# Performance work log

Measured on AMD Instinct MI355X. Metric: run time of the kernel, lower is better.

## Reference

```python
import jax, jax.numpy as jnp
import numpy as np

BATCH = 4
N_MELS, T_LEN, PATCH = 128, 512, 16
D_MODEL, D_INNER, D_STATE, DT_RANK, D_CONV = 512, 1024, 16, 32, 4
DEPTH, N_CLASSES = 4, 10


def _silu(x):
    return x * jax.nn.sigmoid(x)


def _ln(x, w, b):
    m = x.mean(-1, keepdims=True)
    v = ((x - m) ** 2).mean(-1, keepdims=True)
    return (x - m) * jax.lax.rsqrt(v + 1e-5) * w + b


def _causal_conv(x, w, b):
    # x: (B, L, D); w: (D, K) depthwise causal conv (mamba conv1d)
    K, L = w.shape[-1], x.shape[1]
    xp = jnp.pad(x, ((0, 0), (K - 1, 0), (0, 0)))
    y = sum(xp[:, k:k + L, :] * w[:, k] for k in range(K))
    return y + b


def _ssm(xc, conv_w, conv_b, xproj_w, dtproj_w, dtproj_b, A_log, Dp):
    # One directional selective scan (mamba S6).
    u = _silu(_causal_conv(xc, conv_w, conv_b))              # (B,L,Di)
    xdbl = jnp.einsum('bld,ed->ble', u, xproj_w)             # (B,L,dt_rank+2S)
    dtr, Bm, Cm = jnp.split(xdbl, [DT_RANK, DT_RANK + D_STATE], axis=-1)
    dt = jax.nn.softplus(jnp.einsum('blr,dr->bld', dtr, dtproj_w) + dtproj_b)
    A = -jnp.exp(A_log)                                      # (Di,S)
    dA = jnp.exp(dt[..., None] * A)                          # (B,L,Di,S)
    dBu = (dt * u)[..., None] * Bm[:, :, None, :]            # (B,L,Di,S)

    def comb(e1, e2):
        a1, b1 = e1
        a2, b2 = e2
        return a1 * a2, a2 * b1 + b2

    _, h = jax.lax.associative_scan(comb, (dA, dBu), axis=1)  # parallel linear recurrence
    return jnp.einsum('blds,bls->bld', h, Cm) + u * Dp


def _forward(x, patch_w, patch_b, in_proj_w, conv_w_f, conv_b_f, conv_w_b, conv_b_b,
             xproj_w_f, xproj_w_b, dtproj_w_f, dtproj_b_f, dtproj_w_b, dtproj_b_b,
             A_log_f, A_log_b, D_f, D_b, out_proj_w, norm_w, norm_b,
             normf_w, normf_b, ln_w, ln_b, fc1_w, fc1_b, fc2_w, fc2_b):
    B = x.shape[0]
    # Patch embed: conv with kernel == stride -> reshape + einsum
    xp = x.reshape(B, 1, N_MELS // PATCH, PATCH, T_LEN // PATCH, PATCH)
    tok = jnp.einsum('bchpwq,dcpq->bhwd', xp, patch_w) + patch_b
    h = tok.reshape(B, -1, D_MODEL)                           # (B, 256, D)
    for i in range(DEPTH):
        xn = _ln(h, norm_w[i], norm_b[i])
        xz = jnp.einsum('bld,ed->ble', xn, in_proj_w[i])
        xc, z = jnp.split(xz, 2, axis=-1)
        y_f = _ssm(xc, conv_w_f[i], conv_b_f[i], xproj_w_f[i],
                   dtproj_w_f[i], dtproj_b_f[i], A_log_f[i], D_f[i])
        y_b = jnp.flip(_ssm(jnp.flip(xc, 1), conv_w_b[i], conv_b_b[i], xproj_w_b[i],
                            dtproj_w_b[i], dtproj_b_b[i], A_log_b[i], D_b[i]), 1)
        y = (y_f + y_b) * _silu(z)                            # bimamba v2: fwd + flipped bwd, gated
        h = h + jnp.einsum('bld,ed->ble', y, out_proj_w[i])
    h = _ln(h, normf_w, normf_b)
    feat = h.mean(axis=1)                                     # pooled features (B, D)
    c = _ln(feat, ln_w, ln_b)
    c = jnp.maximum(c @ fc1_w.T + fc1_b, 0.0)
    return c @ fc2_w.T + fc2_b


def setup_inputs() -> dict:
    ks = iter(jax.random.split(jax.random.key(0), 64))

    def rn(shape, s=0.02):
        return jax.random.normal(next(ks), shape, jnp.float32) * s

    inp = {}
    inp['x'] = jax.random.normal(next(ks), (BATCH, 1, N_MELS, T_LEN), jnp.float32)
    inp['patch_w'] = rn((D_MODEL, 1, PATCH, PATCH))
    inp['patch_b'] = jnp.zeros((D_MODEL,), jnp.float32)
    inp['in_proj_w'] = rn((DEPTH, 2 * D_INNER, D_MODEL))
    A_init = jnp.log(jnp.tile(jnp.arange(1, D_STATE + 1, dtype=jnp.float32), (DEPTH, D_INNER, 1)))
    for sfx in ('f', 'b'):
        inp[f'conv_w_{sfx}'] = rn((DEPTH, D_INNER, D_CONV), 0.2)
        inp[f'conv_b_{sfx}'] = jnp.zeros((DEPTH, D_INNER), jnp.float32)
        inp[f'xproj_w_{sfx}'] = rn((DEPTH, DT_RANK + 2 * D_STATE, D_INNER))
        inp[f'dtproj_w_{sfx}'] = rn((DEPTH, D_INNER, DT_RANK), 0.1)
        inp[f'dtproj_b_{sfx}'] = jnp.full((DEPTH, D_INNER), -4.6, jnp.float32)  # softplus -> dt ~ 0.01
        inp[f'A_log_{sfx}'] = A_init
        inp[f'D_{sfx}'] = jnp.ones((DEPTH, D_INNER), jnp.float32)
    inp['out_proj_w'] = rn((DEPTH, D_MODEL, D_INNER))
    inp['norm_w'] = jnp.ones((DEPTH, D_MODEL), jnp.float32)
    inp['norm_b'] = jnp.zeros((DEPTH, D_MODEL), jnp.float32)
    inp['normf_w'] = jnp.ones((D_MODEL,), jnp.float32)
    inp['normf_b'] = jnp.zeros((D_MODEL,), jnp.float32)
    inp['ln_w'] = jnp.ones((D_MODEL,), jnp.float32)
    inp['ln_b'] = jnp.zeros((D_MODEL,), jnp.float32)
    inp['fc1_w'] = rn((512, D_MODEL))
    inp['fc1_b'] = jnp.zeros((512,), jnp.float32)
    inp['fc2_w'] = rn((N_CLASSES, 512))
    inp['fc2_b'] = jnp.zeros((N_CLASSES,), jnp.float32)
    return inp


def reference(x, patch_w, patch_b, in_proj_w, conv_w_f, conv_b_f, conv_w_b, conv_b_b,
              xproj_w_f, xproj_w_b, dtproj_w_f, dtproj_b_f, dtproj_w_b, dtproj_b_b,
              A_log_f, A_log_b, D_f, D_b, out_proj_w, norm_w, norm_b,
              normf_w, normf_b, ln_w, ln_b, fc1_w, fc1_b, fc2_w, fc2_b):
    return _forward(x, patch_w, patch_b, in_proj_w, conv_w_f, conv_b_f, conv_w_b, conv_b_b,
                    xproj_w_f, xproj_w_b, dtproj_w_f, dtproj_b_f, dtproj_w_b, dtproj_b_b,
                    A_log_f, A_log_b, D_f, D_b, out_proj_w, norm_w, norm_b,
                    normf_w, normf_b, ln_w, ln_b, fc1_w, fc1_b, fc2_w, fc2_b)
```

## Files before the change

### kernel.cpp

```cpp
#include <hip/hip_runtime.h>


#define BB 4
#define LL 256
#define DM 512
#define DI 1024

typedef unsigned short u16;
typedef unsigned int u32;
typedef __attribute__((ext_vector_type(8))) short s8v;
typedef __attribute__((ext_vector_type(4))) float f4v;

__device__ __forceinline__ float silu_f(float x){ return x/(1.f+__expf(-x)); }
__device__ __forceinline__ float b2f(u16 u){
  union { u32 i; float f; } v; v.i = ((u32)u) << 16; return v.f;
}
__device__ __forceinline__ u16 f2bf(float f){
  union { float f; u32 u; } v; v.f = f;
  u32 r = (v.u + 0x7fffu + ((v.u >> 16) & 1u)) >> 16;
  return (u16)r;
}
__device__ __forceinline__ void split8(const float* f, s8v& hi, s8v& lo){
#pragma unroll
  for (int j = 0; j < 8; ++j){
    u16 h = f2bf(f[j]);
    float hf = b2f(h);
    hi[j] = (short)h;
    lo[j] = (short)f2bf(f[j] - hf);
  }
}

__device__ __forceinline__ float row_sum16(float p){
  union { float f; int i; } v, r;
  v.f = p;
  r.i = __builtin_amdgcn_update_dpp(0, v.i, 0x111, 0xF, 0xF, true); v.f += r.f;
  r.i = __builtin_amdgcn_update_dpp(0, v.i, 0x112, 0xF, 0xF, true); v.f += r.f;
  r.i = __builtin_amdgcn_update_dpp(0, v.i, 0x114, 0xF, 0xF, true); v.f += r.f;
  r.i = __builtin_amdgcn_update_dpp(0, v.i, 0x118, 0xF, 0xF, true); v.f += r.f;
  return v.f;
}

__device__ __forceinline__ void block_reduce2(float& a, float& b, float* sc, int nw){
  int lane = threadIdx.x & 63, wid = threadIdx.x >> 6;
#pragma unroll
  for (int o = 32; o > 0; o >>= 1){
    a += __shfl_down(a, o, 64);
    b += __shfl_down(b, o, 64);
  }
  if (lane == 0){ sc[wid*2] = a; sc[wid*2+1] = b; }
  __syncthreads();
  float ta = 0.f, tb = 0.f;
  for (int i = 0; i < nw; ++i){ ta += sc[i*2]; tb += sc[i*2+1]; }
  a = ta; b = tb;
}

__global__ __launch_bounds__(256) void convert_w(const float* __restrict__ inW,
    const float* __restrict__ outW, u16* __restrict__ inHi, u16* __restrict__ inLo,
    u16* __restrict__ outHi, u16* __restrict__ outLo){
  int idx = blockIdx.x*256 + threadIdx.x;
  const float4* src; ushort4* dh; ushort4* dl;
  if (idx < 262144){
    src = (const float4*)inW + idx;
    dh = (ushort4*)inHi + idx; dl = (ushort4*)inLo + idx;
  } else {
    int j = idx - 262144;
    src = (const float4*)outW + j;
    dh = (ushort4*)outHi + j; dl = (ushort4*)outLo + j;
  }
  float4 v = *src;
  ushort4 h, l;
  h.x = f2bf(v.x); l.x = f2bf(v.x - b2f(h.x));
  h.y = f2bf(v.y); l.y = f2bf(v.y - b2f(h.y));
  h.z = f2bf(v.z); l.z = f2bf(v.z - b2f(h.z));
  h.w = f2bf(v.w); l.w = f2bf(v.w - b2f(h.w));
  *dh = h; *dl = l;
}

__global__ __launch_bounds__(256) void patch_embed(const float* __restrict__ x,
    const float* __restrict__ pw, const float* __restrict__ pb, float* __restrict__ h){
  __shared__ float xs[8*256];
  int blk = blockIdx.x;
  int b = blk >> 6, ph = (blk >> 3) & 7, pg = (blk >> 1) & 3, dh = blk & 1;
  int t = threadIdx.x;
  for (int idx = t; idx < 2048; idx += 256){
    int j = idx >> 8, pix = idx & 255, p = pix >> 4, q = pix & 15;
    xs[idx] = x[(size_t)(b*128 + ph*16 + p)*512 + pg*128 + j*16 + q];
  }
  __syncthreads();
  int d = dh*256 + t;
  float acc[8] = {};
  const float* wr = pw + (size_t)d*256;
  for (int i = 0; i < 256; i += 8){
    float4 w0 = *(const float4*)(wr + i);
    float4 w1 = *(const float4*)(wr + i + 4);
    float wf[8] = {w0.x,w0.y,w0.z,w0.w,w1.x,w1.y,w1.z,w1.w};
#pragma unroll
    for (int j = 0; j < 8; ++j){
#pragma unroll
      for (int jj = 0; jj < 8; ++jj)
        acc[j] = fmaf(xs[j*256 + i + jj], wf[jj], acc[j]);
    }
  }
  float bias = pb[d];
#pragma unroll
  for (int j = 0; j < 8; ++j)
    h[(size_t)(b*256 + ph*32 + pg*8 + j)*512 + d] = acc[j] + bias;
}

__global__ __launch_bounds__(256) void gemm1_ln_mfma(const float* __restrict__ X,
    const float* __restrict__ lnw, const float* __restrict__ lnb, int lnOff,
    const u16* __restrict__ Whi, const u16* __restrict__ Wlo, float* __restrict__ C){
  __shared__ __align__(16) u16 Ah[2048], Al[2048], Bh[2048], Bl[2048];
  __shared__ float rmean[64], rrstd[64];
  int bm = blockIdx.y*64, bn = blockIdx.x*64;
  int t = threadIdx.x;
  int sr = t >> 2, sc = (t & 3)*8;
  {
    const float* xr = X + (size_t)(bm + sr)*512 + (t & 3)*128;
    float s = 0.f, ss = 0.f;
    for (int i = 0; i < 128; i += 4){
      float4 v = *(const float4*)(xr + i);
      s  += v.x + v.y + v.z + v.w;
      ss += v.x*v.x + v.y*v.y + v.z*v.z + v.w*v.w;
    }
    s += __shfl_xor(s, 1, 64); ss += __shfl_xor(ss, 1, 64);
    s += __shfl_xor(s, 2, 64); ss += __shfl_xor(ss, 2, 64);
    if ((t & 3) == 0){
      float m = s * (1.f/512.f);
      float var = ss * (1.f/512.f) - m*m;
      rmean[sr] = m; rrstd[sr] = rsqrtf(var + 1e-5f);
    }
  }
  __syncthreads();
  float mm = rmean[sr], rr = rrstd[sr];
  int lane = t & 63, wv = t >> 6, ml = lane & 15, quad = lane >> 4;
  int mq = wv >> 1, nq = wv & 1;
  f4v acc[2][2] = {};
  for (int k0 = 0; k0 < 512; k0 += 32){
    const float* xr = X + (size_t)(bm + sr)*512 + k0 + sc;
    float4 a0 = *(const float4*)xr;
    float4 a1 = *(const float4*)(xr + 4);
    float4 g0 = *(const float4*)(lnw + lnOff + k0 + sc);
    float4 g1 = *(const float4*)(lnw + lnOff + k0 + sc + 4);
    float4 c0 = *(const float4*)(lnb + lnOff + k0 + sc);
    float4 c1 = *(const float4*)(lnb + lnOff + k0 + sc + 4);
    float af[8] = {
      (a0.x-mm)*rr*g0.x + c0.x, (a0.y-mm)*rr*g0.y + c0.y,
      (a0.z-mm)*rr*g0.z + c0.z, (a0.w-mm)*rr*g0.w + c0.w,
      (a1.x-mm)*rr*g1.x + c1.x, (a1.y-mm)*rr*g1.y + c1.y,
      (a1.z-mm)*rr*g1.z + c1.z, (a1.w-mm)*rr*g1.w + c1.w };
    s8v ahv, alv; split8(af, ahv, alv);
    *(s8v*)&Ah[sr*32 + sc] = ahv;
    *(s8v*)&Al[sr*32 + sc] = alv;
    uint4 bhv = *(const uint4*)(Whi + (size_t)(bn + sr)*512 + k0 + sc);
    uint4 blv = *(const uint4*)(Wlo + (size_t)(bn + sr)*512 + k0 + sc);
    *(uint4*)&Bh[sr*32 + sc] = bhv;
    *(uint4*)&Bl[sr*32 + sc] = blv;
    __syncthreads();
    s8v ah[2], al2[2], bh2[2], bl2[2];
#pragma unroll
    for (int mt = 0; mt < 2; ++mt){
      int row = mq*32 + mt*16 + ml;
      ah[mt]  = *(s8v*)&Ah[row*32 + quad*8];
      al2[mt] = *(s8v*)&Al[row*32 + quad*8];
    }
#pragma unroll
    for (int nt = 0; nt < 2; ++nt){
      int col = nq*32 + nt*16 + ml;
      bh2[nt] = *(s8v*)&Bh[col*32 + quad*8];
      bl2[nt] = *(s8v*)&Bl[col*32 + quad*8];
    }
#pragma unroll
    for (int mt = 0; mt < 2; ++mt)
#pragma unroll
      for (int nt = 0; nt < 2; ++nt){
        acc[mt][nt] = __builtin_amdgcn_mfma_f32_16x16x32_bf16(ah[mt],  bh2[nt], acc[mt][nt], 0, 0, 0);
        acc[mt][nt] = __builtin_amdgcn_mfma_f32_16x16x32_bf16(al2[mt], bh2[nt], acc[mt][nt], 0, 0, 0);
        acc[mt][nt] = __builtin_amdgcn_mfma_f32_16x16x32_bf16(ah[mt],  bl2[nt], acc[mt][nt], 0, 0, 0);
      }
    __syncthreads();
  }
#pragma unroll
  for (int mt = 0; mt < 2; ++mt)
#pragma unroll
    for (int nt = 0; nt < 2; ++nt)
#pragma unroll
      for (int r = 0; r < 4; ++r)
        C[(size_t)(bm + mq*32 + mt*16 + quad*4 + r)*2048 + bn + nq*32 + nt*16 + ml] =
            acc[mt][nt][r];
}

__global__ __launch_bounds__(256) void gemm2_gate_mfma(const float* __restrict__ yb2,
    const float* __restrict__ xz, const u16* __restrict__ Whi,
    const u16* __restrict__ Wlo, float* __restrict__ C){
  __shared__ __align__(16) u16 Ah[2048], Al[2048], Bh[2048], Bl[2048];
  int bm = blockIdx.y*64, bn = blockIdx.x*64;
  int t = threadIdx.x;
  int sr = t >> 2, sc = (t & 3)*8;
  int lane = t & 63, wv = t >> 6, ml = lane & 15, quad = lane >> 4;
  int mq = wv >> 1, nq = wv & 1;
  f4v acc[2][2] = {};
  for (int k0 = 0; k0 < 1024; k0 += 32){
    int m = bm + sr;
    const float* fp = yb2 + (size_t)m*DI + k0 + sc;
    const float* rp = yb2 + (size_t)(1024 + m)*DI + k0 + sc;
    const float* zp = xz + (size_t)m*2048 + 1024 + k0 + sc;
    float4 f0 = *(const float4*)fp,       f1 = *(const float4*)(fp + 4);
    float4 r0 = *(const float4*)rp,       r1 = *(const float4*)(rp + 4);
    float4 z0 = *(const float4*)zp,       z1 = *(const float4*)(zp + 4);
    float af[8] = {
      (f0.x+r0.x)*silu_f(z0.x), (f0.y+r0.y)*silu_f(z0.y),
      (f0.z+r0.z)*silu_f(z0.z), (f0.w+r0.w)*silu_f(z0.w),
      (f1.x+r1.x)*silu_f(z1.x), (f1.y+r1.y)*silu_f(z1.y),
      (f1.z+r1.z)*silu_f(z1.z), (f1.w+r1.w)*silu_f(z1.w) };
    s8v ahv, alv; split8(af, ahv, alv);
    *(s8v*)&Ah[sr*32 + sc] = ahv;
    *(s8v*)&Al[sr*32 + sc] = alv;
    uint4 bhv = *(const uint4*)(Whi + (size_t)(bn + sr)*1024 + k0 + sc);
    uint4 blv = *(const uint4*)(Wlo + (size_t)(bn + sr)*1024 + k0 + sc);
    *(uint4*)&Bh[sr*32 + sc] = bhv;
    *(uint4*)&Bl[sr*32 + sc] = blv;
    __syncthreads();
    s8v ah[2], al2[2], bh2[2], bl2[2];
#pragma unroll
    for (int mt = 0; mt < 2; ++mt){
      int row = mq*32 + mt*16 + ml;
      ah[mt]  = *(s8v*)&Ah[row*32 + quad*8];
      al2[mt] = *(s8v*)&Al[row*32 + quad*8];
    }
#pragma unroll
    for (int nt = 0; nt < 2; ++nt){
      int col = nq*32 + nt*16 + ml;
      bh2[nt] = *(s8v*)&Bh[col*32 + quad*8];
      bl2[nt] = *(s8v*)&Bl[col*32 + quad*8];
    }
#pragma unroll
    for (int mt = 0; mt < 2; ++mt)
#pragma unroll
      for (int nt = 0; nt < 2; ++nt){
        acc[mt][nt] = __builtin_amdgcn_mfma_f32_16x16x32_bf16(ah[mt],  bh2[nt], acc[mt][nt], 0, 0, 0);
        acc[mt][nt] = __builtin_amdgcn_mfma_f32_16x16x32_bf16(al2[mt], bh2[nt], acc[mt][nt], 0, 0, 0);
        acc[mt][nt] = __builtin_amdgcn_mfma_f32_16x16x32_bf16(ah[mt],  bl2[nt], acc[mt][nt], 0, 0, 0);
      }
    __syncthreads();
  }
#pragma unroll
  for (int mt = 0; mt < 2; ++mt)
#pragma unroll
    for (int nt = 0; nt < 2; ++nt)
#pragma unroll
      for (int r = 0; r < 4; ++r){
        float* cp = C + (size_t)(bm + mq*32 + mt*16 + quad*4 + r)*512 +
                    bn + nq*32 + nt*16 + ml;
        *cp += acc[mt][nt][r];
      }
}

__global__ __launch_bounds__(256) void fused_cxd(const float* __restrict__ xz,
    const float* __restrict__ cwF, const float* __restrict__ cbF,
    const float* __restrict__ cwB, const float* __restrict__ cbB,
    const float* __restrict__ xwF, const float* __restrict__ xwB,
    const float* __restrict__ dtwF, const float* __restrict__ dtbF,
    const float* __restrict__ dtwB, const float* __restrict__ dtbB,
    int cwOff, int cbOff, int xwOff, int dtwOff, int dtbOff,
    float* __restrict__ u, float* __restrict__ xdbl, float* __restrict__ dtout){
  __shared__ float us[4*1024];
  __shared__ float part[16*64];
  __shared__ float dtr[4*32];
  int blk = blockIdx.x;
  int dir = blk >> 8, rem = blk & 255, b = rem >> 6, lg = rem & 63;
  int l0 = lg*4;
  const float* cw  = dir ? cwB  : cwF;
  const float* cb  = dir ? cbB  : cbF;
  const float* xw  = dir ? xwB  : xwF;
  const float* dtw = dir ? dtwB : dtwF;
  const float* dtb = dir ? dtbB : dtbF;
  int t = threadIdx.x;
  int rbase = (dir*BB + b)*LL;
  for (int dd = 0; dd < 4; ++dd){
    int d = t + dd*256;
    float4 w4 = *(const float4*)(cw + cwOff + d*4);
    float wf[4] = {w4.x, w4.y, w4.z, w4.w};
    float bias = cb[cbOff + d];
#pragma unroll
    for (int r = 0; r < 4; ++r){
      int l = l0 + r;
      float acc = bias;
#pragma unroll
      for (int k = 0; k < 4; ++k){
        int li = l + k - 3;
        if (li >= 0){
          int sl = dir ? (LL-1-li) : li;
          acc = fmaf(xz[(size_t)(b*LL + sl)*2048 + d], wf[k], acc);
        }
      }
      float uval = silu_f(acc);
      us[r*1024 + d] = uval;
      u[(size_t)(rbase + l)*DI + d] = uval;
    }
  }
  __syncthreads();
  {
    int e = t & 63, pr = t >> 6;
    float accs[4] = {};
    const float* wr = xw + xwOff + (size_t)e*1024 + pr*256;
    for (int i = 0; i < 256; i += 8){
      float4 w0 = *(const float4*)(wr + i);
      float4 w1 = *(const float4*)(wr + i + 4);
      float wf[8] = {w0.x,w0.y,w0.z,w0.w,w1.x,w1.y,w1.z,w1.w};
#pragma unroll
      for (int r = 0; r < 4; ++r){
        const float* ub = us + r*1024 + pr*256 + i;
#pragma unroll
        for (int j = 0; j < 8; ++j)
          accs[r] = fmaf(ub[j], wf[j], accs[r]);
      }
    }
#pragma unroll
    for (int r = 0; r < 4; ++r) part[(pr*4 + r)*64 + e] = accs[r];
  }
  __syncthreads();
  {
    int r = t >> 6, e = t & 63;
    float v = part[(0*4+r)*64+e] + part[(1*4+r)*64+e] +
              part[(2*4+r)*64+e] + part[(3*4+r)*64+e];
    xdbl[(size_t)(rbase + l0 + r)*64 + e] = v;
    if (e < 32) dtr[r*32 + e] = v;
  }
  __syncthreads();
  for (int dd = 0; dd < 4; ++dd){
    int d = t + dd*256;
    float bias = dtb[dtbOff + d];
    float accs[4] = {bias, bias, bias, bias};
    const float* wr = dtw + dtwOff + (size_t)d*32;
    for (int i = 0; i < 32; i += 8){
      float4 w0 = *(const float4*)(wr + i);
      float4 w1 = *(const float4*)(wr + i + 4);
      float wf[8] = {w0.x,w0.y,w0.z,w0.w,w1.x,w1.y,w1.z,w1.w};
#pragma unroll
      for (int r = 0; r < 4; ++r)
#pragma unroll
        for (int j = 0; j < 8; ++j)
          accs[r] = fmaf(dtr[r*32 + i + j], wf[j], accs[r]);
    }
#pragma unroll
    for (int r = 0; r < 4; ++r){
      float sv = accs[r];
      dtout[(size_t)(rbase + l0 + r)*DI + d] = (sv > 15.f) ? sv : log1pf(__expf(sv));
    }
  }
}

__global__ __launch_bounds__(256) void scan_coal(const float* __restrict__ dt,
    const float* __restrict__ u, const float* __restrict__ xd,
    const float* __restrict__ AlogF, const float* __restrict__ AlogB,
    const float* __restrict__ DF, const float* __restrict__ DB,
    int aOff, int dOff, float* __restrict__ y){
  __shared__ __align__(16) float dtuT[16][516];
  __shared__ __align__(16) float BCT[16][516];
  __shared__ __align__(16) float ytile[128][16];
  int blk = blockIdx.x;
  int dir = blk >> 8, b = (blk >> 6) & 3, dg = blk & 63;
  int t = threadIdx.x;
  int rbase = (dir*BB + b)*LL;
  const float* Alog = dir ? AlogB : AlogF;
  const float* Dpt  = dir ? DB : DF;
  {
    int q = t & 3, lb = t >> 2;
    for (int pass = 0; pass < 4; ++pass){
      int l = pass*64 + lb;
      float4 dv = *(const float4*)(dt + (size_t)(rbase + l)*DI + dg*16 + q*4);
      float4 uv = *(const float4*)(u  + (size_t)(rbase + l)*DI + dg*16 + q*4);
      float2 p0 = {dv.x, uv.x}, p1 = {dv.y, uv.y}, p2 = {dv.z, uv.z}, p3 = {dv.w, uv.w};
      *(float2*)&dtuT[q*4+0][l*2] = p0;
      *(float2*)&dtuT[q*4+1][l*2] = p1;
      *(float2*)&dtuT[q*4+2][l*2] = p2;
      *(float2*)&dtuT[q*4+3][l*2] = p3;
    }
  }
  {
    int h8 = t & 7, lb = t >> 3;
    for (int pass = 0; pass < 8; ++pass){
      int l = pass*32 + lb;
      float4 v = *(const float4*)(xd + (size_t)(rbase + l)*64 + 32 + h8*4);
      if (h8 < 4){
        int s0 = h8*4;
        BCT[s0+0][l*2] = v.x; BCT[s0+1][l*2] = v.y;
        BCT[s0+2][l*2] = v.z; BCT[s0+3][l*2] = v.w;
      } else {
        int s0 = (h8-4)*4;
        BCT[s0+0][l*2+1] = v.x; BCT[s0+1][l*2+1] = v.y;
        BCT[s0+2][l*2+1] = v.z; BCT[s0+3][l*2+1] = v.w;
      }
    }
  }
  int s = t & 15, dl = t >> 4;
  float Av = -__expf(Alog[aOff + dg*256 + t]);
  float Dp = Dpt[dOff + dg*16 + dl];
  __syncthreads();
  float h = 0.f;
  for (int half = 0; half < 2; ++half){
    for (int l0 = half*128; l0 < half*128 + 128; l0 += 4){
      float4 du01 = *(const float4*)&dtuT[dl][l0*2];
      float4 du23 = *(const float4*)&dtuT[dl][l0*2 + 4];
      float4 bc01 = *(const float4*)&BCT[s][l0*2];
      float4 bc23 = *(const float4*)&BCT[s][l0*2 + 4];
      float dtv[4] = {du01.x, du01.z, du23.x, du23.z};
      float uv[4]  = {du01.y, du01.w, du23.y, du23.w};
      float Bv[4]  = {bc01.x, bc01.z, bc23.x, bc23.z};
      float Cv[4]  = {bc01.y, bc01.w, bc23.y, bc23.w};
#pragma unroll
      for (int i = 0; i < 4; ++i){
        float a = __expf(dtv[i] * Av);
        h = fmaf(a, h, dtv[i]*uv[i]*Bv[i]);
        float p = h * Cv[i];
        float sum = row_sum16(p);
        if (s == 15){
          int lr = (l0 + i) & 127;
          ytile[lr][dl] = fmaf(uv[i], Dp, sum);
        }
      }
    }
    __syncthreads();
    {
      int d4 = t & 3, lh = t >> 2;
      for (int pass = 0; pass < 2; ++pass){
        int lr = pass*64 + lh;
        int l = half*128 + lr;
        int lo = dir ? (255 - l) : l;
        float4 vv = *(const float4*)&ytile[lr][d4*4];
        *(float4*)(y + (size_t)(rbase + lo)*DI + dg*16 + d4*4) = vv;
      }
    }
    __syncthreads();
  }
}

__global__ __launch_bounds__(256) void ln_kernel(const float* __restrict__ x,
    const float* __restrict__ w, const float* __restrict__ bias,
    float* __restrict__ y){
  __shared__ float sc[8];
  int row = blockIdx.x, t = threadIdx.x;
  const float* xr = x + (size_t)row*DM;
  float v0 = xr[t], v1 = xr[t + 256];
  float s = v0 + v1, ss = v0*v0 + v1*v1;
  block_reduce2(s, ss, sc, 4);
  float mean = s * (1.f/512.f);
  float var = ss * (1.f/512.f) - mean*mean;
  float inv = rsqrtf(var + 1e-5f);
  float* yr = y + (size_t)row*DM;
  yr[t]       = (v0 - mean)*inv*w[t]       + bias[t];
  yr[t + 256] = (v1 - mean)*inv*w[t + 256] + bias[t + 256];
}

__global__ __launch_bounds__(256) void pool_kernel(const float* __restrict__ hn,
    float* __restrict__ feat){
  __shared__ float part[4][64];
  int b = blockIdx.x >> 3, dg = blockIdx.x & 7;
  int t = threadIdx.x, dl = t & 63, lq = t >> 6;
  const float* p = hn + (size_t)(b*256 + lq*64)*512 + dg*64 + dl;
  float s = 0.f;
#pragma unroll 4
  for (int i = 0; i < 64; ++i) s += p[(size_t)i*512];
  part[lq][dl] = s;
  __syncthreads();
  if (t < 64)
    feat[b*512 + dg*64 + t] =
        (part[0][t] + part[1][t] + part[2][t] + part[3][t]) * (1.f/256.f);
}

__global__ __launch_bounds__(512) void head_kernel(const float* __restrict__ feat,
    const float* __restrict__ lnw, const float* __restrict__ lnb,
    const float* __restrict__ fc1w, const float* __restrict__ fc1b,
    const float* __restrict__ fc2w, const float* __restrict__ fc2b,
    float* __restrict__ out){
  __shared__ float sc[16];
  __shared__ float cbuf[512];
  __shared__ float rbuf[512];
  int b = blockIdx.x, t = threadIdx.x;
  float v = feat[b*512 + t];
  float s = v, ss = v*v;
  block_reduce2(s, ss, sc, 8);
  float mean = s * (1.f/512.f);
  float var = ss * (1.f/512.f) - mean*mean;
  float inv = rsqrtf(var + 1e-5f);
  cbuf[t] = (v - mean)*inv*lnw[t] + lnb[t];
  __syncthreads();
  float a = fc1b[t];
  const float* w1 = fc1w + (size_t)t*512;
  for (int i = 0; i < 512; i += 8){
    float4 w0 = *(const float4*)(w1 + i);
    float4 w4 = *(const float4*)(w1 + i + 4);
    float wf[8] = {w0.x,w0.y,w0.z,w0.w,w4.x,w4.y,w4.z,w4.w};
#pragma unroll
    for (int j = 0; j < 8; ++j) a = fmaf(cbuf[i + j], wf[j], a);
  }
  rbuf[t] = fmaxf(a, 0.f);
  __syncthreads();
  if (t < 10){
    float a2 = fc2b[t];
    const float* w2 = fc2w + (size_t)t*512;
    for (int i = 0; i < 512; ++i) a2 = fmaf(rbuf[i], w2[i], a2);
    out[b*10 + t] = a2;
  }
}

extern "C" void kernel_launch(void* const* d_in, const int* in_sizes, int n_in,
                              void* d_out, int out_size, void* d_ws, size_t ws_size,
                              hipStream_t stream) {
  (void)in_sizes; (void)n_in; (void)out_size; (void)ws_size;
  const float* x          = (const float*)d_in[0];
  const float* patch_w    = (const float*)d_in[1];
  const float* patch_b    = (const float*)d_in[2];
  const float* in_proj_w  = (const float*)d_in[3];
  const float* conv_w_f   = (const float*)d_in[4];
  const float* conv_b_f   = (const float*)d_in[5];
  const float* xproj_w_f  = (const float*)d_in[6];
  const float* dtproj_w_f = (const float*)d_in[7];
  const float* dtproj_b_f = (const float*)d_in[8];
  const float* A_log_f    = (const float*)d_in[9];
  const float* D_f        = (const float*)d_in[10];
  const float* conv_w_b   = (const float*)d_in[11];
  const float* conv_b_b   = (const float*)d_in[12];
  const float* xproj_w_b  = (const float*)d_in[13];
  const float* dtproj_w_b = (const float*)d_in[14];
  const float* dtproj_b_b = (const float*)d_in[15];
  const float* A_log_b    = (const float*)d_in[16];
  const float* D_b        = (const float*)d_in[17];
  const float* out_proj_w = (const float*)d_in[18];
  const float* norm_w     = (const float*)d_in[19];
  const float* norm_b     = (const float*)d_in[20];
  const float* normf_w    = (const float*)d_in[21];
  const float* normf_b    = (const float*)d_in[22];
  const float* ln_w       = (const float*)d_in[23];
  const float* ln_b       = (const float*)d_in[24];
  const float* fc1_w      = (const float*)d_in[25];
  const float* fc1_b      = (const float*)d_in[26];
  const float* fc2_w      = (const float*)d_in[27];
  const float* fc2_b      = (const float*)d_in[28];

  float* ws   = (float*)d_ws;
  float* hbuf = ws;
  float* xz   = ws + 524288;
  float* ubuf = ws + 2621440;
  float* xdbl = ws + 4718592;
  float* dtb  = ws + 4849664;
  float* ybuf = ws + 6946816;
  float* hn   = ws + 9043968;
  u16*   inHi = (u16*)(ws + 9568256);
  u16*   inLo = (u16*)(ws + 10092544);
  u16*   outHi= (u16*)(ws + 10616832);
  u16*   outLo= (u16*)(ws + 10878976);
  float* feat = ws + 11141120;

  patch_embed<<<256, 256, 0, stream>>>(x, patch_w, patch_b, hbuf);
  for (int i = 0; i < 4; ++i){
    convert_w<<<1536, 256, 0, stream>>>(in_proj_w + (size_t)i*1048576,
                                        out_proj_w + (size_t)i*524288,
                                        inHi, inLo, outHi, outLo);
    gemm1_ln_mfma<<<dim3(32, 16), 256, 0, stream>>>(
        hbuf, norm_w, norm_b, i*512, inHi, inLo, xz);
    fused_cxd<<<512, 256, 0, stream>>>(
        xz, conv_w_f, conv_b_f, conv_w_b, conv_b_b, xproj_w_f, xproj_w_b,
        dtproj_w_f, dtproj_b_f, dtproj_w_b, dtproj_b_b,
        i*4096, i*1024, i*65536, i*32768, i*1024, ubuf, xdbl, dtb);
    scan_coal<<<512, 256, 0, stream>>>(
        dtb, ubuf, xdbl, A_log_f, A_log_b, D_f, D_b, i*16384, i*1024, ybuf);
    gemm2_gate_mfma<<<dim3(8, 16), 256, 0, stream>>>(
        ybuf, xz, outHi, outLo, hbuf);
  }
  ln_kernel<<<1024, 256, 0, stream>>>(hbuf, normf_w, normf_b, hn);
  pool_kernel<<<32, 256, 0, stream>>>(hn, feat);
  head_kernel<<<4, 512, 0, stream>>>(feat, ln_w, ln_b, fc1_w, fc1_b, fc2_w, fc2_b,
                                     (float*)d_out);
}
```

Measured before the change: 756.4 us.

## Split LN and gate prologues into prep kernels, share padded-LDS bf16 GEMM

The LayerNorm and the SiLU gate, along with the hi/lo bf16 split, move out of the two MFMA GEMMs into separate row-wise prep kernels that write bf16 hi/lo activations to workspace. A single generic gemm_bf16 kernel then loads pre-split operands straight into LDS, whose row stride is padded to 40 elements to reduce bank conflicts. This removes the redundant per-tile LN and gate math and bf16 conversion that was repeated across every N-tile block. The cost is two extra launches per layer and an extra round trip of the activations through global memory.

```diff
diff --git a/kernel.cpp b/kernel.cpp
--- a/kernel.cpp
+++ b/kernel.cpp
@@ -5,6 +5,7 @@
 #define LL 256
 #define DM 512
 #define DI 1024
+#define LDST 40
 
 typedef unsigned short u16;
 typedef unsigned int u32;
@@ -19,15 +20,6 @@
   union { float f; u32 u; } v; v.f = f;
   u32 r = (v.u + 0x7fffu + ((v.u >> 16) & 1u)) >> 16;
   return (u16)r;
-}
-__device__ __forceinline__ void split8(const float* f, s8v& hi, s8v& lo){
-#pragma unroll
-  for (int j = 0; j < 8; ++j){
-    u16 h = f2bf(f[j]);
-    float hf = b2f(h);
-    hi[j] = (short)h;
-    lo[j] = (short)f2bf(f[j] - hf);
-  }
 }
 
 __device__ __forceinline__ float row_sum16(float p){
@@ -107,68 +99,76 @@
     h[(size_t)(b*256 + ph*32 + pg*8 + j)*512 + d] = acc[j] + bias;
 }
 
-__global__ __launch_bounds__(256) void gemm1_ln_mfma(const float* __restrict__ X,
-    const float* __restrict__ lnw, const float* __restrict__ lnb, int lnOff,
-    const u16* __restrict__ Whi, const u16* __restrict__ Wlo, float* __restrict__ C){
-  __shared__ __align__(16) u16 Ah[2048], Al[2048], Bh[2048], Bl[2048];
-  __shared__ float rmean[64], rrstd[64];
+__global__ __launch_bounds__(256) void prep_ln(const float* __restrict__ x,
+    const float* __restrict__ w, const float* __restrict__ bias, int wOff,
+    u16* __restrict__ hiO, u16* __restrict__ loO){
+  __shared__ float sc[8];
+  int row = blockIdx.x, t = threadIdx.x;
+  const float* xr = x + (size_t)row*DM;
+  float v0 = xr[t], v1 = xr[t + 256];
+  float s = v0 + v1, ss = v0*v0 + v1*v1;
+  block_reduce2(s, ss, sc, 4);
+  float mean = s * (1.f/512.f);
+  float var = ss * (1.f/512.f) - mean*mean;
+  float inv = rsqrtf(var + 1e-5f);
+  float o0 = (v0 - mean)*inv*w[wOff + t]       + bias[wOff + t];
+  float o1 = (v1 - mean)*inv*w[wOff + t + 256] + bias[wOff + t + 256];
+  u16 h0 = f2bf(o0), h1 = f2bf(o1);
+  hiO[(size_t)row*DM + t]       = h0;
+  hiO[(size_t)row*DM + t + 256] = h1;
+  loO[(size_t)row*DM + t]       = f2bf(o0 - b2f(h0));
+  loO[(size_t)row*DM + t + 256] = f2bf(o1 - b2f(h1));
+}
+
+__global__ __launch_bounds__(256) void prep_gate(const float* __restrict__ ybuf,
+    const float* __restrict__ xz, u16* __restrict__ gHi, u16* __restrict__ gLo){
+  int row = blockIdx.x, t = threadIdx.x;
+  int c = t*4;
+  float4 yf = *(const float4*)(ybuf + (size_t)row*DI + c);
+  float4 yb = *(const float4*)(ybuf + 1048576 + (size_t)row*DI + c);
+  float4 zv = *(const float4*)(xz + (size_t)row*2048 + 1024 + c);
+  float g0 = (yf.x + yb.x)*silu_f(zv.x);
+  float g1 = (yf.y + yb.y)*silu_f(zv.y);
+  float g2 = (yf.z + yb.z)*silu_f(zv.z);
+  float g3 = (yf.w + yb.w)*silu_f(zv.w);
+  ushort4 h, l;
+  h.x = f2bf(g0); l.x = f2bf(g0 - b2f(h.x));
+  h.y = f2bf(g1); l.y = f2bf(g1 - b2f(h.y));
+  h.z = f2bf(g2); l.z = f2bf(g2 - b2f(h.z));
+  h.w = f2bf(g3); l.w = f2bf(g3 - b2f(h.w));
+  *(ushort4*)(gHi + (size_t)row*DI + c) = h;
+  *(ushort4*)(gLo + (size_t)row*DI + c) = l;
+}
+
+__global__ __launch_bounds__(256) void gemm_bf16(const u16* __restrict__ Ahi_g,
+    const u16* __restrict__ Alo_g, int As, const u16* __restrict__ Bhi_g,
+    const u16* __restrict__ Blo_g, int Bs, float* __restrict__ C, int Cs,
+    int K, int addFlag){
+  __shared__ __align__(16) u16 Ah[64*LDST], Al[64*LDST], Bh[64*LDST], Bl[64*LDST];
   int bm = blockIdx.y*64, bn = blockIdx.x*64;
   int t = threadIdx.x;
-  int sr = t >> 2, sc = (t & 3)*8;
-  {
-    const float* xr = X + (size_t)(bm + sr)*512 + (t & 3)*128;
-    float s = 0.f, ss = 0.f;
-    for (int i = 0; i < 128; i += 4){
-      float4 v = *(const float4*)(xr + i);
-      s  += v.x + v.y + v.z + v.w;
-      ss += v.x*v.x + v.y*v.y + v.z*v.z + v.w*v.w;
-    }
-    s += __shfl_xor(s, 1, 64); ss += __shfl_xor(ss, 1, 64);
-    s += __shfl_xor(s, 2, 64); ss += __shfl_xor(ss, 2, 64);
-    if ((t & 3) == 0){
-      float m = s * (1.f/512.f);
-      float var = ss * (1.f/512.f) - m*m;
-      rmean[sr] = m; rrstd[sr] = rsqrtf(var + 1e-5f);
-    }
-  }
-  __syncthreads();
-  float mm = rmean[sr], rr = rrstd[sr];
+  int sr = t >> 2, sc8 = (t & 3)*8;
   int lane = t & 63, wv = t >> 6, ml = lane & 15, quad = lane >> 4;
   int mq = wv >> 1, nq = wv & 1;
   f4v acc[2][2] = {};
-  for (int k0 = 0; k0 < 512; k0 += 32){
-    const float* xr = X + (size_t)(bm + sr)*512 + k0 + sc;
-    float4 a0 = *(const float4*)xr;
-    float4 a1 = *(const float4*)(xr + 4);
-    float4 g0 = *(const float4*)(lnw + lnOff + k0 + sc);
-    float4 g1 = *(const float4*)(lnw + lnOff + k0 + sc + 4);
-    float4 c0 = *(const float4*)(lnb + lnOff + k0 + sc);
-    float4 c1 = *(const float4*)(lnb + lnOff + k0 + sc + 4);
-    float af[8] = {
-      (a0.x-mm)*rr*g0.x + c0.x, (a0.y-mm)*rr*g0.y + c0.y,
-      (a0.z-mm)*rr*g0.z + c0.z, (a0.w-mm)*rr*g0.w + c0.w,
-      (a1.x-mm)*rr*g1.x + c1.x, (a1.y-mm)*rr*g1.y + c1.y,
-      (a1.z-mm)*rr*g1.z + c1.z, (a1.w-mm)*rr*g1.w + c1.w };
-    s8v ahv, alv; split8(af, ahv, alv);
-    *(s8v*)&Ah[sr*32 + sc] = ahv;
-    *(s8v*)&Al[sr*32 + sc] = alv;
-    uint4 bhv = *(const uint4*)(Whi + (size_t)(bn + sr)*512 + k0 + sc);
-    uint4 blv = *(const uint4*)(Wlo + (size_t)(bn + sr)*512 + k0 + sc);
-    *(uint4*)&Bh[sr*32 + sc] = bhv;
-    *(uint4*)&Bl[sr*32 + sc] = blv;
+  for (int k0 = 0; k0 < K; k0 += 32){
+    *(uint4*)&Ah[sr*LDST + sc8] = *(const uint4*)(Ahi_g + (size_t)(bm + sr)*As + k0 + sc8);
+    *(uint4*)&Al[sr*LDST + sc8] = *(const uint4*)(Alo_g + (size_t)(bm + sr)*As + k0 + sc8);
+    *(uint4*)&Bh[sr*LDST + sc8] = *(const uint4*)(Bhi_g + (size_t)(bn + sr)*Bs + k0 + sc8);
+    *(uint4*)&Bl[sr*LDST + sc8] = *(const uint4*)(Blo_g + (size_t)(bn + sr)*Bs + k0 + sc8);
     __syncthreads();
     s8v ah[2], al2[2], bh2[2], bl2[2];
 #pragma unroll
     for (int mt = 0; mt < 2; ++mt){
       int row = mq*32 + mt*16 + ml;
-      ah[mt]  = *(s8v*)&Ah[row*32 + quad*8];
-      al2[mt] = *(s8v*)&Al[row*32 + quad*8];
+      ah[mt]  = *(s8v*)&Ah[row*LDST + quad*8];
+      al2[mt] = *(s8v*)&Al[row*LDST + quad*8];
     }
 #pragma unroll
     for (int nt = 0; nt < 2; ++nt){
       int col = nq*32 + nt*16 + ml;
-      bh2[nt] = *(s8v*)&Bh[col*32 + quad*8];
-      bl2[nt] = *(s8v*)&Bl[col*32 + quad*8];
+      bh2[nt] = *(s8v*)&Bh[col*LDST + quad*8];
+      bl2[nt] = *(s8v*)&Bl[col*LDST + quad*8];
     }
 #pragma unroll
     for (int mt = 0; mt < 2; ++mt)
@@ -185,74 +185,11 @@
 #pragma unroll
     for (int nt = 0; nt < 2; ++nt)
 #pragma unroll
-      for (int r = 0; r < 4; ++r)
-        C[(size_t)(bm + mq*32 + mt*16 + quad*4 + r)*2048 + bn + nq*32 + nt*16 + ml] =
-            acc[mt][nt][r];
-}
-
-__global__ __launch_bounds__(256) void gemm2_gate_mfma(const float* __restrict__ yb2,
-    const float* __restrict__ xz, const u16* __restrict__ Whi,
-    const u16* __restrict__ Wlo, float* __restrict__ C){
-  __shared__ __align__(16) u16 Ah[2048], Al[2048], Bh[2048], Bl[2048];
-  int bm = blockIdx.y*64, bn = blockIdx.x*64;
-  int t = threadIdx.x;
-  int sr = t >> 2, sc = (t & 3)*8;
-  int lane = t & 63, wv = t >> 6, ml = lane & 15, quad = lane >> 4;
-  int mq = wv >> 1, nq = wv & 1;
-  f4v acc[2][2] = {};
-  for (int k0 = 0; k0 < 1024; k0 += 32){
-    int m = bm + sr;
-    const float* fp = yb2 + (size_t)m*DI + k0 + sc;
-    const float* rp = yb2 + (size_t)(1024 + m)*DI + k0 + sc;
-    const float* zp = xz + (size_t)m*2048 + 1024 + k0 + sc;
-    float4 f0 = *(const float4*)fp,       f1 = *(const float4*)(fp + 4);
-    float4 r0 = *(const float4*)rp,       r1 = *(const float4*)(rp + 4);
-    float4 z0 = *(const float4*)zp,       z1 = *(const float4*)(zp + 4);
-    float af[8] = {
-      (f0.x+r0.x)*silu_f(z0.x), (f0.y+r0.y)*silu_f(z0.y),
-      (f0.z+r0.z)*silu_f(z0.z), (f0.w+r0.w)*silu_f(z0.w),
-      (f1.x+r1.x)*silu_f(z1.x), (f1.y+r1.y)*silu_f(z1.y),
-      (f1.z+r1.z)*silu_f(z1.z), (f1.w+r1.w)*silu_f(z1.w) };
-    s8v ahv, alv; split8(af, ahv, alv);
-    *(s8v*)&Ah[sr*32 + sc] = ahv;
-    *(s8v*)&Al[sr*32 + sc] = alv;
-    uint4 bhv = *(const uint4*)(Whi + (size_t)(bn + sr)*1024 + k0 + sc);
-    uint4 blv = *(const uint4*)(Wlo + (size_t)(bn + sr)*1024 + k0 + sc);
-    *(uint4*)&Bh[sr*32 + sc] = bhv;
-    *(uint4*)&Bl[sr*32 + sc] = blv;
-    __syncthreads();
-    s8v ah[2], al2[2], bh2[2], bl2[2];
-#pragma unroll
-    for (int mt = 0; mt < 2; ++mt){
-      int row = mq*32 + mt*16 + ml;
-      ah[mt]  = *(s8v*)&Ah[row*32 + quad*8];
-      al2[mt] = *(s8v*)&Al[row*32 + quad*8];
-    }
-#pragma unroll
-    for (int nt = 0; nt < 2; ++nt){
-      int col = nq*32 + nt*16 + ml;
-      bh2[nt] = *(s8v*)&Bh[col*32 + quad*8];
-      bl2[nt] = *(s8v*)&Bl[col*32 + quad*8];
-    }
-#pragma unroll
-    for (int mt = 0; mt < 2; ++mt)
-#pragma unroll
-      for (int nt = 0; nt < 2; ++nt){
-        acc[mt][nt] = __builtin_amdgcn_mfma_f32_16x16x32_bf16(ah[mt],  bh2[nt], acc[mt][nt], 0, 0, 0);
-        acc[mt][nt] = __builtin_amdgcn_mfma_f32_16x16x32_bf16(al2[mt], bh2[nt], acc[mt][nt], 0, 0, 0);
-        acc[mt][nt] = __builtin_amdgcn_mfma_f32_16x16x32_bf16(ah[mt],  bl2[nt], acc[mt][nt], 0, 0, 0);
-      }
-    __syncthreads();
-  }
-#pragma unroll
-  for (int mt = 0; mt < 2; ++mt)
-#pragma unroll
-    for (int nt = 0; nt < 2; ++nt)
-#pragma unroll
       for (int r = 0; r < 4; ++r){
-        float* cp = C + (size_t)(bm + mq*32 + mt*16 + quad*4 + r)*512 +
+        float* cp = C + (size_t)(bm + mq*32 + mt*16 + quad*4 + r)*Cs +
                     bn + nq*32 + nt*16 + ml;
-        *cp += acc[mt][nt][r];
+        if (addFlag) *cp += acc[mt][nt][r];
+        else         *cp  = acc[mt][nt][r];
       }
 }
 
@@ -552,22 +489,28 @@
   u16*   outHi= (u16*)(ws + 10616832);
   u16*   outLo= (u16*)(ws + 10878976);
   float* feat = ws + 11141120;
+  u16*   xnHi = (u16*)hn;
+  u16*   xnLo = (u16*)(ws + 9043968 + 262144);
+  u16*   gHi  = (u16*)ubuf;
+  u16*   gLo  = (u16*)(ws + 2621440 + 524288);
 
   patch_embed<<<256, 256, 0, stream>>>(x, patch_w, patch_b, hbuf);
   for (int i = 0; i < 4; ++i){
     convert_w<<<1536, 256, 0, stream>>>(in_proj_w + (size_t)i*1048576,
                                         out_proj_w + (size_t)i*524288,
                                         inHi, inLo, outHi, outLo);
-    gemm1_ln_mfma<<<dim3(32, 16), 256, 0, stream>>>(
-        hbuf, norm_w, norm_b, i*512, inHi, inLo, xz);
+    prep_ln<<<1024, 256, 0, stream>>>(hbuf, norm_w, norm_b, i*512, xnHi, xnLo);
+    gemm_bf16<<<dim3(32, 16), 256, 0, stream>>>(
+        xnHi, xnLo, 512, inHi, inLo, 512, xz, 2048, 512, 0);
     fused_cxd<<<512, 256, 0, stream>>>(
         xz, conv_w_f, conv_b_f, conv_w_b, conv_b_b, xproj_w_f, xproj_w_b,
         dtproj_w_f, dtproj_b_f, dtproj_w_b, dtproj_b_b,
         i*4096, i*1024, i*65536, i*32768, i*1024, ubuf, xdbl, dtb);
     scan_coal<<<512, 256, 0, stream>>>(
         dtb, ubuf, xdbl, A_log_f, A_log_b, D_f, D_b, i*16384, i*1024, ybuf);
-    gemm2_gate_mfma<<<dim3(8, 16), 256, 0, stream>>>(
-        ybuf, xz, outHi, outLo, hbuf);
+    prep_gate<<<1024, 256, 0, stream>>>(ybuf, xz, gHi, gLo);
+    gemm_bf16<<<dim3(8, 16), 256, 0, stream>>>(
+        gHi, gLo, 1024, outHi, outLo, 1024, hbuf, 512, 1024, 1);
   }
   ln_kernel<<<1024, 256, 0, stream>>>(hbuf, normf_w, normf_b, hn);
   pool_kernel<<<32, 256, 0, stream>>>(hn, feat);
```

Measured after the change: 664.2 us. 1.14x faster.
